# Kernel tuning notes

Measured on AMD Instinct MI355X. Metric: run time of the kernel, lower is better.

Reference implementation:

```python
import jax, jax.numpy as jnp
import numpy as np

MAX_NODES = 8192
MAX_EDGES = 16384
D = 64
NEG = -1e10


def setup_inputs() -> dict:
    key = jax.random.key(0)
    k1, k2, k3, k4, k5, k6 = jax.random.split(key, 6)
    N, E = MAX_NODES, MAX_EDGES
    nodes = jax.random.normal(k1, (N, D), jnp.float32)
    edges = jax.random.normal(k2, (E, D), jnp.float32)
    receivers = jax.random.randint(k3, (E,), 0, N, jnp.int32)
    senders = jax.random.randint(k4, (E,), 0, N, jnp.int32)
    active_nodes = jnp.ones((N,), jnp.float32)
    active_edges = (jnp.arange(E) < E // 4).astype(jnp.float32)  # prefix of active edges
    Wq = jax.random.normal(k5, (D, D), jnp.float32) / jnp.sqrt(jnp.float32(D))
    Wp = jax.random.normal(k6, (D, 1), jnp.float32) * 0.05
    bq = jnp.zeros((D,), jnp.float32)
    bp = jnp.full((1,), -4.0, jnp.float32)
    return dict(nodes=nodes, edges=edges, receivers=receivers, senders=senders,
                active_nodes=active_nodes, active_edges=active_edges,
                Wq=Wq, bq=bq, Wp=Wp, bp=bp)


def _incr_edges(aedges, n):
    # Closed form of n steps of x <- clip(x @ (I + superdiag), 0, 1):
    # out[j] = 1 iff any(aedges[j-n : j+1]) != 0, then last slot forced to 0.
    c = jnp.cumsum(aedges)
    idx = jnp.arange(aedges.shape[0])
    prev = jnp.where(idx - n - 1 >= 0, c[jnp.clip(idx - n - 1, 0)], 0.0)
    out = ((c - prev) > 0).astype(aedges.dtype)
    return out.at[-1].set(0.0)


def reference(nodes, edges, receivers, senders, active_nodes, active_edges, Wq, bq, Wp, bp):
    N, E = MAX_NODES, MAX_EDGES
    key = jax.random.key(42)
    key_prob, key_edges, key_samp = jax.random.split(key, 3)
    nids = jnp.arange(N)
    e_active = active_edges.sum().astype(jnp.int32)

    # 1-2. edge-generation probability per node + Bernoulli sampling of generators
    probs = jax.nn.sigmoid(nodes @ Wp + bp)[:, 0]                       # [N]
    gens = (jax.random.uniform(key_prob, (N,)) < probs * active_nodes).astype(jnp.float32)

    # 3-4. queries and pairwise cosine-similarity scores[i, j] = cos(q_i, h_j)
    queries = nodes @ Wq + bq                                           # [N, D]
    num = queries @ nodes.T                                             # [N, N]
    qn = jnp.sum(queries * queries, -1)                                 # [N]
    hn = jnp.sum(nodes * nodes, -1)                                     # [N]
    scores = num / (jnp.sqrt(qn[:, None] * hn[None, :]) + 1e-8)
    scores = jnp.clip(scores, -10000.0, 10000.0)
    scores = jnp.where(active_nodes[None, :] > 0, scores, NEG)
    gens = gens * (scores.max(-1) > -jnp.inf).astype(jnp.float32)       # threshold = -inf
    scores = jnp.where(jnp.eye(N, dtype=bool), NEG, scores)             # no self-loops

    # 5. sample target j* per generating node (softmax mode)
    select = jnp.where(gens > 0, jax.random.categorical(key_samp, scores, axis=-1), 0)

    # drop generators whose edge (i, j*) already exists
    is_s = nids[:, None] == senders[None, :]                            # [N, E]
    is_r = select[:, None] == receivers[None, :]                        # [N, E]
    exist = jnp.logical_and(is_s, is_r).any(-1) & (gens > 0)
    gens = jnp.where(exist, 0.0, gens)

    # 6. scatter new edges into the fixed-size buffers
    allowed = E - e_active - 1
    n_gens = jnp.clip(gens.astype(jnp.int32).sum(), 0, allowed)
    naedges = _incr_edges(active_edges, n_gens)
    mask_new = naedges * (1.0 - active_edges)                           # [E]
    new_edges = edges + jax.random.normal(key_edges, edges.shape) * mask_new[:, None]

    t1 = (jnp.cumsum(gens) * gens - 1.0).astype(jnp.int32) + (e_active * gens).astype(jnp.int32)
    nsend = jax.ops.segment_sum(nids, t1, E)
    nsend = jnp.where(mask_new > 0, nsend, senders)

    t2 = jnp.cumsum(gens) * gens - gens
    t2 = jnp.where(gens > 0, t2.astype(jnp.int32), -1) + (e_active * gens).astype(jnp.int32)
    nrec = jax.ops.segment_sum(select, t2, E)
    nrec = jnp.where(mask_new > 0, nrec, receivers)

    nrec = jnp.where(naedges > 0, nrec, N - 1)
    nsend = jnp.where(naedges > 0, nsend, N - 1)
    return new_edges, nsend, nrec, naedges
```

## Files before the change

kernel.cpp:

```cpp
#include <hip/hip_runtime.h>
#include <stdint.h>

#define NN 8192
#define NE 16384
#define DD 64
#define GCAP 512
#define SLICES 32
#define NEGV -1e10f
#define TINYF 1.17549435e-38f
#define SQRT2F 1.41421356237f

__device__ __forceinline__ uint2 tf2x32(uint32_t k0, uint32_t k1, uint32_t x0, uint32_t x1) {
  uint32_t ks2 = k0 ^ k1 ^ 0x1BD11BDAu;
  x0 += k0; x1 += k1;
#define TF_R(r) { x0 += x1; x1 = (x1 << (r)) | (x1 >> (32 - (r))); x1 ^= x0; }
  TF_R(13) TF_R(15) TF_R(26) TF_R(6)
  x0 += k1; x1 += ks2 + 1u;
  TF_R(17) TF_R(29) TF_R(16) TF_R(24)
  x0 += ks2; x1 += k0 + 2u;
  TF_R(13) TF_R(15) TF_R(26) TF_R(6)
  x0 += k0; x1 += k1 + 3u;
  TF_R(17) TF_R(29) TF_R(16) TF_R(24)
  x0 += k1; x1 += ks2 + 4u;
  TF_R(13) TF_R(15) TF_R(26) TF_R(6)
  x0 += ks2; x1 += k0 + 5u;
#undef TF_R
  return make_uint2(x0, x1);
}
__device__ __forceinline__ uint2 jax_subkey(uint32_t i) { return tf2x32(0u, 42u, 0u, i); }
__device__ __forceinline__ uint32_t rbits(uint2 k, uint32_t idx) {
  uint2 r = tf2x32(k.x, k.y, 0u, idx);
  return r.x ^ r.y;
}
__device__ __forceinline__ float u01f(uint32_t b) {
  return __uint_as_float((b >> 9) | 0x3F800000u) - 1.0f;
}
__device__ __forceinline__ float erfinv_xla(float x) {
  float w = -log1pf(-x * x);
  float p;
  if (w < 5.0f) {
    w -= 2.5f;
    p = 2.81022636e-08f;
    p = fmaf(p, w, 3.43273939e-07f);
    p = fmaf(p, w, -3.5233877e-06f);
    p = fmaf(p, w, -4.39150654e-06f);
    p = fmaf(p, w, 0.00021858087f);
    p = fmaf(p, w, -0.00125372503f);
    p = fmaf(p, w, -0.00417768164f);
    p = fmaf(p, w, 0.246640727f);
    p = fmaf(p, w, 1.50140941f);
  } else {
    w = sqrtf(w) - 3.0f;
    p = -0.000200214257f;
    p = fmaf(p, w, 0.000100950558f);
    p = fmaf(p, w, 0.00134934322f);
    p = fmaf(p, w, -0.00367342844f);
    p = fmaf(p, w, 0.00573950773f);
    p = fmaf(p, w, -0.0076224613f);
    p = fmaf(p, w, 0.00943887047f);
    p = fmaf(p, w, 1.00167406f);
    p = fmaf(p, w, 2.83297682f);
  }
  return p * x;
}
__device__ __forceinline__ float jax_normal(uint2 k, uint32_t idx) {
  float f = u01f(rbits(k, idx));
  float lo = __uint_as_float(0xBF7FFFFFu);
  float u = fmaxf(lo, f * 2.0f + lo);
  return SQRT2F * erfinv_xla(u);
}
__device__ __forceinline__ float jax_gumbel(uint2 k, uint32_t idx) {
  float f = u01f(rbits(k, idx));
  float u = fmaxf(TINYF, f + TINYF);
  return -logf(-logf(u));
}


__global__ void sg_gens(const float* __restrict__ nodes, const float* __restrict__ Wp,
                        const float* __restrict__ bp, const float* __restrict__ anodes,
                        int* __restrict__ gens0, float* __restrict__ hn) {
  int lane = threadIdx.x & 63;
  int i = blockIdx.x * 4 + (threadIdx.x >> 6);
  float v = nodes[i * DD + lane];
  float ss = v * v;
  float dp = v * Wp[lane];
  for (int off = 32; off > 0; off >>= 1) {
    ss += __shfl_xor(ss, off, 64);
    dp += __shfl_xor(dp, off, 64);
  }
  if (lane == 0) {
    hn[i] = ss;
    float x = dp + bp[0];
    float p = 1.0f / (1.0f + expf(-x));
    uint2 kp = jax_subkey(0u);
    float u = u01f(rbits(kp, (uint32_t)i));
    gens0[i] = (u < p * anodes[i]) ? 1 : 0;
  }
}

__global__ void sg_scan(const float* __restrict__ aedges, const int* __restrict__ gens0,
                        int* __restrict__ c, int* __restrict__ gidx, int* __restrict__ sc) {
  __shared__ int ts[256];
  int t = threadIdx.x;
  int base = t * 64;
  uint64_t bits = 0;
  int s = 0;
  const float4* a4 = (const float4*)(aedges + base);
  for (int k4 = 0; k4 < 16; k4++) {
    float4 v = a4[k4];
    if (v.x != 0.0f) { bits |= 1ull << (4 * k4 + 0); s++; }
    if (v.y != 0.0f) { bits |= 1ull << (4 * k4 + 1); s++; }
    if (v.z != 0.0f) { bits |= 1ull << (4 * k4 + 2); s++; }
    if (v.w != 0.0f) { bits |= 1ull << (4 * k4 + 3); s++; }
  }
  ts[t] = s;
  __syncthreads();
  for (int off = 1; off < 256; off <<= 1) {
    int add = (t >= off) ? ts[t - off] : 0;
    __syncthreads();
    ts[t] += add;
    __syncthreads();
  }
  int run = ts[t] - s;
  for (int k = 0; k < 64; k++) {
    run += (int)((bits >> k) & 1ull);
    c[base + k] = run;
  }
  if (t == 255) { sc[1] = ts[255]; sc[2] = NE - ts[255] - 1; }
  __syncthreads();
  int b2 = t * 32;
  uint32_t gb = 0;
  int s2 = 0;
  const int4* g4 = (const int4*)(gens0 + b2);
  for (int k4 = 0; k4 < 8; k4++) {
    int4 v = g4[k4];
    if (v.x) { gb |= 1u << (4 * k4 + 0); s2++; }
    if (v.y) { gb |= 1u << (4 * k4 + 1); s2++; }
    if (v.z) { gb |= 1u << (4 * k4 + 2); s2++; }
    if (v.w) { gb |= 1u << (4 * k4 + 3); s2++; }
  }
  ts[t] = s2;
  __syncthreads();
  for (int off = 1; off < 256; off <<= 1) {
    int add = (t >= off) ? ts[t - off] : 0;
    __syncthreads();
    ts[t] += add;
    __syncthreads();
  }
  int r = ts[t] - s2;
  for (int k = 0; k < 32; k++)
    if ((gb >> k) & 1u) gidx[r++] = b2 + k;
  if (t == 255) sc[0] = ts[255];
}

__global__ __launch_bounds__(256) void sg_part(
    const float* __restrict__ nodes, const float* __restrict__ anodes,
    const float* __restrict__ hn, const int* __restrict__ gidx,
    const int* __restrict__ sc, const float* __restrict__ Wq,
    const float* __restrict__ bq, float* __restrict__ party,
    int* __restrict__ partj) {
  __shared__ float sq[4][DD];
  __shared__ float sqn[4];
  __shared__ int si[4];
  __shared__ float wy[4][4];
  __shared__ int wj[4][4];
  int G = min(sc[0], GCAP);
  int nGq = (G + 3) >> 2;
  int total = nGq * SLICES;
  int t = threadIdx.x;
  int wid = t >> 6, lane = t & 63;
  uint2 ks = jax_subkey(2u);
  for (int item = blockIdx.x; item < total; item += gridDim.x) {
    int gq = item >> 5, s = item & 31;
    int g0 = gq * 4;
    __syncthreads();
    if (t < 4) { int g = g0 + t; si[t] = (g < G) ? gidx[g] : -1; }
    __syncthreads();
    if (t < DD) {
      int i0 = si[0] < 0 ? 0 : si[0];
      int i1 = si[1] < 0 ? 0 : si[1];
      int i2 = si[2] < 0 ? 0 : si[2];
      int i3 = si[3] < 0 ? 0 : si[3];
      float a0 = bq[t], a1 = a0, a2 = a0, a3 = a0;
      for (int k = 0; k < DD; k++) {
        float w = Wq[k * DD + t];
        a0 = fmaf(nodes[i0 * DD + k], w, a0);
        a1 = fmaf(nodes[i1 * DD + k], w, a1);
        a2 = fmaf(nodes[i2 * DD + k], w, a2);
        a3 = fmaf(nodes[i3 * DD + k], w, a3);
      }
      sq[0][t] = a0; sq[1][t] = a1; sq[2][t] = a2; sq[3][t] = a3;
      float s0 = a0 * a0, s1 = a1 * a1, s2 = a2 * a2, s3 = a3 * a3;
      for (int off = 32; off > 0; off >>= 1) {
        s0 += __shfl_xor(s0, off, 64);
        s1 += __shfl_xor(s1, off, 64);
        s2 += __shfl_xor(s2, off, 64);
        s3 += __shfl_xor(s3, off, 64);
      }
      if (t == 0) { sqn[0] = s0; sqn[1] = s1; sqn[2] = s2; sqn[3] = s3; }
    }
    __syncthreads();
    int j = s * 256 + t;
    float4 nv[16];
    const float4* np4 = (const float4*)(nodes + (size_t)j * DD);
    for (int k4 = 0; k4 < 16; k4++) nv[k4] = np4[k4];
    float hnj = hn[j];
    float act = anodes[j];
    float yy[4];
    for (int u = 0; u < 4; u++) {
      int iu = si[u];
      if (iu < 0) { yy[u] = -INFINITY; continue; }
      float num = 0.0f;
      for (int k4 = 0; k4 < 16; k4++) {
        const float4 qv = *(const float4*)&sq[u][4 * k4];
        num += nv[k4].x * qv.x + nv[k4].y * qv.y + nv[k4].z * qv.z + nv[k4].w * qv.w;
      }
      float denom = sqrtf(sqn[u] * hnj) + 1e-8f;
      float sco = num / denom;
      sco = fminf(fmaxf(sco, -10000.0f), 10000.0f);
      if (!(act > 0.0f)) sco = NEGV;
      if (j == iu) sco = NEGV;
      yy[u] = sco + jax_gumbel(ks, (uint32_t)iu * (uint32_t)NN + (uint32_t)j);
    }
    for (int u = 0; u < 4; u++) {
      float y = yy[u];
      int bj = j;
      for (int off = 32; off > 0; off >>= 1) {
        float oy = __shfl_xor(y, off, 64);
        int oj = __shfl_xor(bj, off, 64);
        if (oy > y || (oy == y && oj < bj)) { y = oy; bj = oj; }
      }
      if (lane == 0) { wy[u][wid] = y; wj[u][wid] = bj; }
    }
    __syncthreads();
    if (t < 4) {
      int u = t;
      if (g0 + u < G) {
        float y = wy[u][0];
        int bj = wj[u][0];
        for (int w = 1; w < 4; w++) {
          if (wy[u][w] > y || (wy[u][w] == y && wj[u][w] < bj)) { y = wy[u][w]; bj = wj[u][w]; }
        }
        party[(g0 + u) * SLICES + s] = y;
        partj[(g0 + u) * SLICES + s] = bj;
      }
    }
  }
}

__global__ void sg_sel(const int* __restrict__ sc, const float* __restrict__ party,
                       const int* __restrict__ partj, const int* __restrict__ gidx,
                       const int* __restrict__ senders, const int* __restrict__ receivers,
                       int* __restrict__ sel, int* __restrict__ keptf) {
  int g = blockIdx.x;
  int G = min(sc[0], GCAP);
  if (g >= G) return;
  int t = threadIdx.x;
  __shared__ int js_s;
  __shared__ int ex;
  if (t < 64) {
    float y = (t < SLICES) ? party[g * SLICES + t] : -INFINITY;
    int bj = (t < SLICES) ? partj[g * SLICES + t] : 0x7fffffff;
    for (int off = 32; off > 0; off >>= 1) {
      float oy = __shfl_xor(y, off, 64);
      int oj = __shfl_xor(bj, off, 64);
      if (oy > y || (oy == y && oj < bj)) { y = oy; bj = oj; }
    }
    if (t == 0) { js_s = bj; ex = 0; }
  }
  __syncthreads();
  int i = gidx[g], js = js_s;
  int f = 0;
  for (int e = t; e < NE; e += 256)
    f |= (senders[e] == i && receivers[e] == js) ? 1 : 0;
  if (f) ex = 1;
  __syncthreads();
  if (t == 0) { sel[g] = js; keptf[g] = ex ? 0 : 1; }
}

__global__ void sg_rank(const int* __restrict__ gidx, const int* __restrict__ sel,
                        const int* __restrict__ keptf, int* __restrict__ sc,
                        int* __restrict__ fid, int* __restrict__ fsel) {
  __shared__ int ts[256];
  int t = threadIdx.x;
  int G = min(sc[0], GCAP);
  int base = t * 32;
  int s = 0;
  for (int k = 0; k < 32; k++) { int g = base + k; if (g < G) s += keptf[g]; }
  ts[t] = s;
  __syncthreads();
  for (int off = 1; off < 256; off <<= 1) {
    int add = (t >= off) ? ts[t - off] : 0;
    __syncthreads();
    ts[t] += add;
    __syncthreads();
  }
  int r = ts[t] - s;
  for (int k = 0; k < 32; k++) {
    int g = base + k;
    if (g < G && keptf[g]) { fid[r] = gidx[g]; fsel[r] = sel[g]; r++; }
  }
  if (t == 255) {
    int kt = ts[255];
    int allowed = sc[2];
    int ng = kt > 0 ? kt : 0;
    if (ng > allowed) ng = allowed;
    sc[3] = kt; sc[4] = ng;
  }
}

__global__ void sg_write(const float* __restrict__ edges, const float* __restrict__ aedges,
                         const int* __restrict__ senders, const int* __restrict__ receivers,
                         const int* __restrict__ c, const int* __restrict__ sc,
                         const int* __restrict__ fid, const int* __restrict__ fsel,
                         float* __restrict__ out_edges, float* __restrict__ out_send,
                         float* __restrict__ out_rec, float* __restrict__ out_na) {
  int t4 = blockIdx.x * 256 + threadIdx.x;
  float4 v = ((const float4*)edges)[t4];
  int e = t4 >> 4;
  int n = sc[4];
  int ce = c[e];
  int pidx = e - n - 1;
  int prev = (pidx >= 0) ? c[pidx] : 0;
  int na = ((ce - prev) > 0 && e != NE - 1) ? 1 : 0;
  float mv = na ? (1.0f - aedges[e]) : 0.0f;
  if (mv != 0.0f) {
    uint2 ke = jax_subkey(1u);
    uint32_t b = (uint32_t)t4 * 4u;
    v.x += jax_normal(ke, b + 0u) * mv;
    v.y += jax_normal(ke, b + 1u) * mv;
    v.z += jax_normal(ke, b + 2u) * mv;
    v.w += jax_normal(ke, b + 3u) * mv;
  }
  ((float4*)out_edges)[t4] = v;
  if ((t4 & 15) == 0) {
    int ea = sc[1], kept = sc[3];
    float ns, nr;
    if (!na) {
      ns = nr = (float)(NN - 1);
    } else if (mv > 0.0f) {
      int r = e - ea;
      bool ok = (r >= 0 && r < kept);
      ns = ok ? (float)fid[r] : 0.0f;
      nr = ok ? (float)fsel[r] : 0.0f;
    } else {
      ns = (float)senders[e];
      nr = (float)receivers[e];
    }
    out_send[e] = ns;
    out_rec[e] = nr;
    out_na[e] = (float)na;
  }
}

extern "C" void kernel_launch(void* const* d_in, const int* in_sizes, int n_in,
                              void* d_out, int out_size, void* d_ws, size_t ws_size,
                              hipStream_t stream) {
  const float* nodes     = (const float*)d_in[0];
  const float* edges     = (const float*)d_in[1];
  const int*   receivers = (const int*)d_in[2];
  const int*   senders   = (const int*)d_in[3];
  const float* anodes    = (const float*)d_in[4];
  const float* aedges    = (const float*)d_in[5];
  const float* Wq        = (const float*)d_in[6];
  const float* bq        = (const float*)d_in[7];
  const float* Wp        = (const float*)d_in[8];
  const float* bp        = (const float*)d_in[9];

  float* out       = (float*)d_out;
  float* out_edges = out;
  float* out_send  = out + (size_t)NE * DD;
  float* out_rec   = out_send + NE;
  float* out_na    = out_rec + NE;

  int* sc     = (int*)d_ws;
  int* gens0  = sc + 8;
  int* gidx   = gens0 + NN;
  int* sel    = gidx + NN;
  int* keptf  = sel + GCAP;
  int* fid    = keptf + GCAP;
  int* fsel   = fid + GCAP;
  int* c      = fsel + GCAP;
  int* partj  = c + NE;
  float* hn   = (float*)(partj + GCAP * SLICES);
  float* party= hn + NN;

  sg_gens  <<<NN / 4, 256, 0, stream>>>(nodes, Wp, bp, anodes, gens0, hn);
  sg_scan  <<<1, 256, 0, stream>>>(aedges, gens0, c, gidx, sc);
  sg_part  <<<2048, 256, 0, stream>>>(nodes, anodes, hn, gidx, sc, Wq, bq, party, partj);
  sg_sel   <<<GCAP, 256, 0, stream>>>(sc, party, partj, gidx, senders, receivers, sel, keptf);
  sg_rank  <<<1, 256, 0, stream>>>(gidx, sel, keptf, sc, fid, fsel);
  sg_write <<<NE * DD / 4 / 256, 256, 0, stream>>>(edges, aedges, senders, receivers, c, sc,
                                                   fid, fsel, out_edges, out_send, out_rec,
                                                   out_na);
}
```

Before: 150.8 us.

## Fuse scan, selection and ranking stages into fewer kernels with atomic completion counters

Folds the single-block edge scan into the node-gating kernel as an extra block, and builds the generator index list with an atomicAdd instead of a second scan. The partial-score kernel now also runs the per-group argmax and duplicate-edge check, using a last-arriving-block counter per group of four generators. A further global counter picks the block that does the final ranking. This cuts the launch count and removes serial single-block kernels from the critical path, but adds atomics, fences, a memset of the counters, and an atomic ordering of generator slots that is nondeterministic.

```diff
diff --git a/kernel.cpp b/kernel.cpp
--- a/kernel.cpp
+++ b/kernel.cpp
@@ -5,6 +5,7 @@
 #define NE 16384
 #define DD 64
 #define GCAP 512
+#define GQCAP 128
 #define SLICES 32
 #define NEGV -1e10f
 #define TINYF 1.17549435e-38f
@@ -74,11 +75,46 @@
   float u = fmaxf(TINYF, f + TINYF);
   return -logf(-logf(u));
 }
-
-
-__global__ void sg_gens(const float* __restrict__ nodes, const float* __restrict__ Wp,
-                        const float* __restrict__ bp, const float* __restrict__ anodes,
-                        int* __restrict__ gens0, float* __restrict__ hn) {
+__device__ __forceinline__ int aload(int* p) {
+  return __hip_atomic_load(p, __ATOMIC_ACQUIRE, __HIP_MEMORY_SCOPE_AGENT);
+}
+
+
+__global__ void sg_front(const float* __restrict__ nodes, const float* __restrict__ Wp,
+                         const float* __restrict__ bp, const float* __restrict__ anodes,
+                         const float* __restrict__ aedges, int* __restrict__ sc,
+                         int* __restrict__ gens0, int* __restrict__ gidx,
+                         int* __restrict__ c, float* __restrict__ hn) {
+  if (blockIdx.x == NN / 4) {
+    __shared__ int ts[256];
+    int t = threadIdx.x;
+    int base = t * 64;
+    uint64_t bits = 0;
+    int s = 0;
+    const float4* a4 = (const float4*)(aedges + base);
+    for (int k4 = 0; k4 < 16; k4++) {
+      float4 v = a4[k4];
+      if (v.x != 0.0f) { bits |= 1ull << (4 * k4 + 0); s++; }
+      if (v.y != 0.0f) { bits |= 1ull << (4 * k4 + 1); s++; }
+      if (v.z != 0.0f) { bits |= 1ull << (4 * k4 + 2); s++; }
+      if (v.w != 0.0f) { bits |= 1ull << (4 * k4 + 3); s++; }
+    }
+    ts[t] = s;
+    __syncthreads();
+    for (int off = 1; off < 256; off <<= 1) {
+      int add = (t >= off) ? ts[t - off] : 0;
+      __syncthreads();
+      ts[t] += add;
+      __syncthreads();
+    }
+    int run = ts[t] - s;
+    for (int k = 0; k < 64; k++) {
+      run += (int)((bits >> k) & 1ull);
+      c[base + k] = run;
+    }
+    if (t == 255) { sc[1] = ts[255]; sc[2] = NE - ts[255] - 1; }
+    return;
+  }
   int lane = threadIdx.x & 63;
   int i = blockIdx.x * 4 + (threadIdx.x >> 6);
   float v = nodes[i * DD + lane];
@@ -94,84 +130,48 @@
     float p = 1.0f / (1.0f + expf(-x));
     uint2 kp = jax_subkey(0u);
     float u = u01f(rbits(kp, (uint32_t)i));
-    gens0[i] = (u < p * anodes[i]) ? 1 : 0;
-  }
-}
-
-__global__ void sg_scan(const float* __restrict__ aedges, const int* __restrict__ gens0,
-                        int* __restrict__ c, int* __restrict__ gidx, int* __restrict__ sc) {
-  __shared__ int ts[256];
-  int t = threadIdx.x;
-  int base = t * 64;
-  uint64_t bits = 0;
-  int s = 0;
-  const float4* a4 = (const float4*)(aedges + base);
-  for (int k4 = 0; k4 < 16; k4++) {
-    float4 v = a4[k4];
-    if (v.x != 0.0f) { bits |= 1ull << (4 * k4 + 0); s++; }
-    if (v.y != 0.0f) { bits |= 1ull << (4 * k4 + 1); s++; }
-    if (v.z != 0.0f) { bits |= 1ull << (4 * k4 + 2); s++; }
-    if (v.w != 0.0f) { bits |= 1ull << (4 * k4 + 3); s++; }
-  }
-  ts[t] = s;
-  __syncthreads();
-  for (int off = 1; off < 256; off <<= 1) {
-    int add = (t >= off) ? ts[t - off] : 0;
-    __syncthreads();
-    ts[t] += add;
-    __syncthreads();
-  }
-  int run = ts[t] - s;
-  for (int k = 0; k < 64; k++) {
-    run += (int)((bits >> k) & 1ull);
-    c[base + k] = run;
-  }
-  if (t == 255) { sc[1] = ts[255]; sc[2] = NE - ts[255] - 1; }
-  __syncthreads();
-  int b2 = t * 32;
-  uint32_t gb = 0;
-  int s2 = 0;
-  const int4* g4 = (const int4*)(gens0 + b2);
-  for (int k4 = 0; k4 < 8; k4++) {
-    int4 v = g4[k4];
-    if (v.x) { gb |= 1u << (4 * k4 + 0); s2++; }
-    if (v.y) { gb |= 1u << (4 * k4 + 1); s2++; }
-    if (v.z) { gb |= 1u << (4 * k4 + 2); s2++; }
-    if (v.w) { gb |= 1u << (4 * k4 + 3); s2++; }
-  }
-  ts[t] = s2;
-  __syncthreads();
-  for (int off = 1; off < 256; off <<= 1) {
-    int add = (t >= off) ? ts[t - off] : 0;
-    __syncthreads();
-    ts[t] += add;
-    __syncthreads();
-  }
-  int r = ts[t] - s2;
-  for (int k = 0; k < 32; k++)
-    if ((gb >> k) & 1u) gidx[r++] = b2 + k;
-  if (t == 255) sc[0] = ts[255];
-}
-
-__global__ __launch_bounds__(256) void sg_part(
+    int g = (u < p * anodes[i]) ? 1 : 0;
+    gens0[i] = g;
+    if (g) {
+      int slot = atomicAdd(&sc[0], 1);
+      if (slot < NN) gidx[slot] = i;
+    }
+  }
+}
+
+__global__ __launch_bounds__(256) void sg_partsel(
     const float* __restrict__ nodes, const float* __restrict__ anodes,
     const float* __restrict__ hn, const int* __restrict__ gidx,
-    const int* __restrict__ sc, const float* __restrict__ Wq,
-    const float* __restrict__ bq, float* __restrict__ party,
-    int* __restrict__ partj) {
+    int* __restrict__ sc, int* __restrict__ slicedone,
+    const float* __restrict__ Wq, const float* __restrict__ bq,
+    const int* __restrict__ senders, const int* __restrict__ receivers,
+    const int* __restrict__ gens0, float* __restrict__ party, int* __restrict__ partj,
+    int* __restrict__ selby, int* __restrict__ keptby,
+    int* __restrict__ fid, int* __restrict__ fsel) {
   __shared__ float sq[4][DD];
   __shared__ float sqn[4];
   __shared__ int si[4];
   __shared__ float wy[4][4];
   __shared__ int wj[4][4];
+  __shared__ int winflag, rankflag;
+  __shared__ int jsout[4];
+  __shared__ int exu[4];
+  __shared__ int ts[256];
   int G = min(sc[0], GCAP);
   int nGq = (G + 3) >> 2;
   int total = nGq * SLICES;
   int t = threadIdx.x;
   int wid = t >> 6, lane = t & 63;
   uint2 ks = jax_subkey(2u);
+  int* partyi = (int*)party;
+
+  if (total == 0) {
+    if (blockIdx.x == 0 && t == 0) { sc[3] = 0; sc[4] = 0; }
+    return;
+  }
+
   for (int item = blockIdx.x; item < total; item += gridDim.x) {
-    int gq = item >> 5, s = item & 31;
+    int gq = item / SLICES, s = item % SLICES;
     int g0 = gq * 4;
     __syncthreads();
     if (t < 4) { int g = g0 + t; si[t] = (g < G) ? gidx[g] : -1; }
@@ -238,74 +238,100 @@
       if (g0 + u < G) {
         float y = wy[u][0];
         int bj = wj[u][0];
-        for (int w = 1; w < 4; w++) {
+        for (int w = 1; w < 4; w++)
           if (wy[u][w] > y || (wy[u][w] == y && wj[u][w] < bj)) { y = wy[u][w]; bj = wj[u][w]; }
-        }
         party[(g0 + u) * SLICES + s] = y;
         partj[(g0 + u) * SLICES + s] = bj;
       }
-    }
-  }
-}
-
-__global__ void sg_sel(const int* __restrict__ sc, const float* __restrict__ party,
-                       const int* __restrict__ partj, const int* __restrict__ gidx,
-                       const int* __restrict__ senders, const int* __restrict__ receivers,
-                       int* __restrict__ sel, int* __restrict__ keptf) {
-  int g = blockIdx.x;
-  int G = min(sc[0], GCAP);
-  if (g >= G) return;
-  int t = threadIdx.x;
-  __shared__ int js_s;
-  __shared__ int ex;
-  if (t < 64) {
-    float y = (t < SLICES) ? party[g * SLICES + t] : -INFINITY;
-    int bj = (t < SLICES) ? partj[g * SLICES + t] : 0x7fffffff;
-    for (int off = 32; off > 0; off >>= 1) {
-      float oy = __shfl_xor(y, off, 64);
-      int oj = __shfl_xor(bj, off, 64);
-      if (oy > y || (oy == y && oj < bj)) { y = oy; bj = oj; }
-    }
-    if (t == 0) { js_s = bj; ex = 0; }
-  }
-  __syncthreads();
-  int i = gidx[g], js = js_s;
-  int f = 0;
-  for (int e = t; e < NE; e += 256)
-    f |= (senders[e] == i && receivers[e] == js) ? 1 : 0;
-  if (f) ex = 1;
-  __syncthreads();
-  if (t == 0) { sel[g] = js; keptf[g] = ex ? 0 : 1; }
-}
-
-__global__ void sg_rank(const int* __restrict__ gidx, const int* __restrict__ sel,
-                        const int* __restrict__ keptf, int* __restrict__ sc,
-                        int* __restrict__ fid, int* __restrict__ fsel) {
-  __shared__ int ts[256];
-  int t = threadIdx.x;
-  int G = min(sc[0], GCAP);
-  int base = t * 32;
-  int s = 0;
-  for (int k = 0; k < 32; k++) { int g = base + k; if (g < G) s += keptf[g]; }
-  ts[t] = s;
-  __syncthreads();
-  for (int off = 1; off < 256; off <<= 1) {
-    int add = (t >= off) ? ts[t - off] : 0;
-    __syncthreads();
-    ts[t] += add;
-    __syncthreads();
-  }
-  int r = ts[t] - s;
-  for (int k = 0; k < 32; k++) {
-    int g = base + k;
-    if (g < G && keptf[g]) { fid[r] = gidx[g]; fsel[r] = sel[g]; r++; }
-  }
-  if (t == 255) {
-    int kt = ts[255];
-    int allowed = sc[2];
-    int ng = kt > 0 ? kt : 0;
-    if (ng > allowed) ng = allowed;
-    sc[3] = kt; sc[4] = ng;
+      __threadfence();
+    }
+    __syncthreads();
+    if (t == 0) {
+      int old = atomicAdd(&slicedone[gq], 1);
+      winflag = (old == SLICES - 1) ? 1 : 0;
+    }
+    __syncthreads();
+    if (winflag) {
+      if (t < 64) {
+        for (int u = 0; u < 4; u++) {
+          if (g0 + u >= G) { if (lane == 0) jsout[u] = 0; continue; }
+          float y; int bj;
+          if (lane < SLICES) {
+            int idx = (g0 + u) * SLICES + lane;
+            y = __int_as_float(aload(&partyi[idx]));
+            bj = aload(&partj[idx]);
+          } else { y = -INFINITY; bj = 0x7fffffff; }
+          for (int off = 32; off > 0; off >>= 1) {
+            float oy = __shfl_xor(y, off, 64);
+            int oj = __shfl_xor(bj, off, 64);
+            if (oy > y || (oy == y && oj < bj)) { y = oy; bj = oj; }
+          }
+          if (lane == 0) jsout[u] = bj;
+        }
+      }
+      if (t < 4) exu[t] = 0;
+      __syncthreads();
+      int i0 = si[0], i1 = si[1], i2 = si[2], i3 = si[3];
+      int j0 = jsout[0], j1 = jsout[1], j2 = jsout[2], j3 = jsout[3];
+      int f0 = 0, f1 = 0, f2 = 0, f3 = 0;
+      for (int e = t; e < NE; e += 256) {
+        int se = senders[e], re = receivers[e];
+        f0 |= (se == i0 && re == j0);
+        f1 |= (se == i1 && re == j1);
+        f2 |= (se == i2 && re == j2);
+        f3 |= (se == i3 && re == j3);
+      }
+      if (f0) exu[0] = 1;
+      if (f1) exu[1] = 1;
+      if (f2) exu[2] = 1;
+      if (f3) exu[3] = 1;
+      __syncthreads();
+      if (t < 4) {
+        if (si[t] >= 0) {
+          selby[si[t]] = jsout[t];
+          keptby[si[t]] = exu[t] ? 0 : 1;
+        }
+        __threadfence();
+      }
+      __syncthreads();
+      if (t == 0) {
+        int old = atomicAdd(&sc[5], 1);
+        rankflag = (old == nGq - 1) ? 1 : 0;
+      }
+      __syncthreads();
+      if (rankflag) {
+        int base = t * (NN / 256);
+        int cnt = 0;
+        for (int k = 0; k < NN / 256; k++) {
+          int id = base + k;
+          if (gens0[id]) cnt += aload(&keptby[id]);
+        }
+        ts[t] = cnt;
+        __syncthreads();
+        for (int off = 1; off < 256; off <<= 1) {
+          int add = (t >= off) ? ts[t - off] : 0;
+          __syncthreads();
+          ts[t] += add;
+          __syncthreads();
+        }
+        int r = ts[t] - cnt;
+        for (int k = 0; k < NN / 256; k++) {
+          int id = base + k;
+          if (gens0[id] && aload(&keptby[id])) {
+            fid[r] = id;
+            fsel[r] = aload(&selby[id]);
+            r++;
+          }
+        }
+        if (t == 255) {
+          int kt = ts[255];
+          int allowed = sc[2];
+          int ng = kt > 0 ? kt : 0;
+          if (ng > allowed) ng = allowed;
+          sc[3] = kt; sc[4] = ng;
+        }
+      }
+    }
   }
 }
 
@@ -373,24 +399,27 @@
   float* out_rec   = out_send + NE;
   float* out_na    = out_rec + NE;
 
-  int* sc     = (int*)d_ws;
-  int* gens0  = sc + 8;
-  int* gidx   = gens0 + NN;
-  int* sel    = gidx + NN;
-  int* keptf  = sel + GCAP;
-  int* fid    = keptf + GCAP;
-  int* fsel   = fid + GCAP;
-  int* c      = fsel + GCAP;
-  int* partj  = c + NE;
-  float* hn   = (float*)(partj + GCAP * SLICES);
-  float* party= hn + NN;
-
-  sg_gens  <<<NN / 4, 256, 0, stream>>>(nodes, Wp, bp, anodes, gens0, hn);
-  sg_scan  <<<1, 256, 0, stream>>>(aedges, gens0, c, gidx, sc);
-  sg_part  <<<2048, 256, 0, stream>>>(nodes, anodes, hn, gidx, sc, Wq, bq, party, partj);
-  sg_sel   <<<GCAP, 256, 0, stream>>>(sc, party, partj, gidx, senders, receivers, sel, keptf);
-  sg_rank  <<<1, 256, 0, stream>>>(gidx, sel, keptf, sc, fid, fsel);
-  sg_write <<<NE * DD / 4 / 256, 256, 0, stream>>>(edges, aedges, senders, receivers, c, sc,
-                                                   fid, fsel, out_edges, out_send, out_rec,
-                                                   out_na);
-}
+  int* sc        = (int*)d_ws;
+  int* slicedone = sc + 16;
+  int* gens0     = slicedone + GQCAP;
+  int* gidx      = gens0 + NN;
+  int* selby     = gidx + NN;
+  int* keptby    = selby + NN;
+  int* fid       = keptby + NN;
+  int* fsel      = fid + GCAP;
+  int* c         = fsel + GCAP;
+  int* partj     = c + NE;
+  float* hn      = (float*)(partj + GCAP * SLICES);
+  float* party   = hn + NN;
+
+  hipMemsetAsync(d_ws, 0, (16 + GQCAP) * sizeof(int), stream);
+
+  sg_front  <<<NN / 4 + 1, 256, 0, stream>>>(nodes, Wp, bp, anodes, aedges, sc, gens0,
+                                             gidx, c, hn);
+  sg_partsel<<<2048, 256, 0, stream>>>(nodes, anodes, hn, gidx, sc, slicedone, Wq, bq,
+                                       senders, receivers, gens0, party, partj, selby,
+                                       keptby, fid, fsel);
+  sg_write  <<<NE * DD / 4 / 256, 256, 0, stream>>>(edges, aedges, senders, receivers, c, sc,
+                                                    fid, fsel, out_edges, out_send, out_rec,
+                                                    out_na);
+}
```

Measured after the change: 217.8 us. 1.44x slower.
